# Kernel optimization log

Measured on AMD Instinct MI355X. Metric: run time of the kernel, lower is better.

The kernel has to match this reference:

```python
import jax, jax.numpy as jnp
import numpy as np

B, L, D, H = 2, 256, 256, 4
DH = D // H  # 64


def setup_inputs() -> dict:
    key = jax.random.key(0)
    ks = jax.random.split(key, 20)
    inp = {
        "q": jax.random.normal(ks[0], (B, L, D), jnp.float32),
        "k": jax.random.normal(ks[1], (B, L, D), jnp.float32),
        "v": jax.random.normal(ks[2], (B, L, D), jnp.float32),
        "attn_mask": jnp.zeros((L, L), jnp.float32),  # nonzero => masked
        "key_padding_mask": jnp.zeros((B, L), bool),
        "pitch_rel": jax.random.normal(ks[3], (B, L, L, D), jnp.float32),
        "dur_rel": jax.random.normal(ks[4], (B, L, L, D), jnp.float32),
    }
    scale = 1.0 / np.sqrt(D)
    names = ["Wq", "Wk", "Wv", "fc", "pr", "dr"]
    for i, n in enumerate(names):
        inp[n + "_w"] = jax.random.normal(ks[5 + 2 * i], (D, D), jnp.float32) * scale
        inp[n + "_b"] = jax.random.normal(ks[6 + 2 * i], (D,), jnp.float32) * 0.01
    return inp


def _linear(x, w, b):
    # torch nn.Linear: y = x @ W^T + b
    return jnp.matmul(x, w.T) + b


def reference(q, k, v, attn_mask, key_padding_mask, pitch_rel, dur_rel,
              Wq_w, Wq_b, Wk_w, Wk_b, Wv_w, Wv_b, fc_w, fc_b,
              pr_w, pr_b, dr_w, dr_b):
    Bq, Lq, Dm = q.shape
    Lk = k.shape[1]
    # project and split heads -> (B, H, L, DH)
    def heads(x, w, b):
        return _linear(x, w, b).reshape(Bq, -1, H, DH).transpose(0, 2, 1, 3)
    qh, kh, vh = heads(q, Wq_w, Wq_b), heads(k, Wk_w, Wk_b), heads(v, Wv_w, Wv_b)

    # content scores: (B, H, Lq, Lk)
    logits = jnp.einsum("bhid,bhjd->bhij", qh, kh)

    # relative pitch bias: pitch_rel (B, Lq, Lk, D) -> (B, Lq, Lk, H, DH)
    pr = _linear(pitch_rel, pr_w, pr_b).reshape(Bq, Lq, Lk, H, DH)
    logits = logits + jnp.einsum("bhid,bijhd->bhij", qh, pr)

    dr = _linear(dur_rel, dr_w, dr_b).reshape(Bq, Lq, Lk, H, DH)
    logits = logits + jnp.einsum("bhid,bijhd->bhij", qh, dr)

    logits = logits / np.sqrt(DH)

    # mask: key_padding_mask broadcast over the QUERY axis (as in source),
    # attn_mask nonzero => masked
    mask = jnp.logical_or(key_padding_mask[:, None, :, None],
                          (attn_mask != 0)[None, None, :, :])
    logits = jnp.where(mask, jnp.float32(-9e15), logits)

    attn = jax.nn.softmax(logits, axis=-1)  # (B, H, Lq, Lk)
    out = jnp.einsum("bhij,bhjd->bhid", attn, vh)  # (B, H, Lq, DH)
    out = out.transpose(0, 2, 1, 3).reshape(Bq, Lq, Dm)
    out = _linear(out, fc_w, fc_b)  # dropout is identity in eval mode
    return out, attn
```

## Files before the change

kernel.cpp:

```cpp
#include <hip/hip_runtime.h>
#include <math.h>


__global__ __launch_bounds__(256) void k_transpose(const float* __restrict__ in,
                                                   float* __restrict__ out) {
  __shared__ float t[32][33];
  int bx = blockIdx.x & 7, by = blockIdx.x >> 3;
  int x = threadIdx.x & 31, y0 = threadIdx.x >> 5;
#pragma unroll
  for (int yy = 0; yy < 32; yy += 8)
    t[yy + y0][x] = in[(size_t)(by * 32 + yy + y0) * 256 + bx * 32 + x];
  __syncthreads();
#pragma unroll
  for (int yy = 0; yy < 32; yy += 8)
    out[(size_t)(bx * 32 + yy + y0) * 256 + by * 32 + x] = t[x][yy + y0];
}

__global__ __launch_bounds__(256) void k_proj(
    const float* __restrict__ q, const float* __restrict__ k_, const float* __restrict__ v,
    const float* __restrict__ Wq, const float* __restrict__ Bq,
    const float* __restrict__ Wk, const float* __restrict__ Bk,
    const float* __restrict__ Wv, const float* __restrict__ Bv,
    float* __restrict__ qh, float* __restrict__ kh, float* __restrict__ vh) {
  int blk = blockIdx.x;
  int m = blk >> 5;
  int r = blk & 31;
  int b = r >> 4, it = (r >> 2) & 3, ot = r & 3;
  const float* X = (m == 0) ? q : (m == 1) ? k_ : v;
  const float* W = (m == 0) ? Wq : (m == 1) ? Wk : Wv;
  const float* Bs = (m == 0) ? Bq : (m == 1) ? Bk : Bv;
  float* OUT = (m == 0) ? qh : (m == 1) ? kh : vh;
  const float scale = (m == 0) ? 0.125f : 1.0f;

  __shared__ float xs[64][33];
  __shared__ float ws[64][33];
  int tid = threadIdx.x;
  int ti = tid >> 4, to = tid & 15;
  int lr = tid >> 2, lc = (tid & 3) * 8;
  float acc[4][4] = {};

  for (int k0 = 0; k0 < 256; k0 += 32) {
    float4 a0 = *(const float4*)(X + (size_t)(b * 256 + it * 64 + lr) * 256 + k0 + lc);
    float4 a1 = *(const float4*)(X + (size_t)(b * 256 + it * 64 + lr) * 256 + k0 + lc + 4);
    xs[lr][lc + 0] = a0.x; xs[lr][lc + 1] = a0.y; xs[lr][lc + 2] = a0.z; xs[lr][lc + 3] = a0.w;
    xs[lr][lc + 4] = a1.x; xs[lr][lc + 5] = a1.y; xs[lr][lc + 6] = a1.z; xs[lr][lc + 7] = a1.w;
    float4 w0 = *(const float4*)(W + (size_t)(ot * 64 + lr) * 256 + k0 + lc);
    float4 w1 = *(const float4*)(W + (size_t)(ot * 64 + lr) * 256 + k0 + lc + 4);
    ws[lr][lc + 0] = w0.x; ws[lr][lc + 1] = w0.y; ws[lr][lc + 2] = w0.z; ws[lr][lc + 3] = w0.w;
    ws[lr][lc + 4] = w1.x; ws[lr][lc + 5] = w1.y; ws[lr][lc + 6] = w1.z; ws[lr][lc + 7] = w1.w;
    __syncthreads();
#pragma unroll
    for (int kk = 0; kk < 32; ++kk) {
      float xv0 = xs[ti * 4 + 0][kk], xv1 = xs[ti * 4 + 1][kk];
      float xv2 = xs[ti * 4 + 2][kk], xv3 = xs[ti * 4 + 3][kk];
      float wv0 = ws[0 * 16 + to][kk], wv1 = ws[1 * 16 + to][kk];
      float wv2 = ws[2 * 16 + to][kk], wv3 = ws[3 * 16 + to][kk];
      acc[0][0] += xv0 * wv0; acc[0][1] += xv0 * wv1; acc[0][2] += xv0 * wv2; acc[0][3] += xv0 * wv3;
      acc[1][0] += xv1 * wv0; acc[1][1] += xv1 * wv1; acc[1][2] += xv1 * wv2; acc[1][3] += xv1 * wv3;
      acc[2][0] += xv2 * wv0; acc[2][1] += xv2 * wv1; acc[2][2] += xv2 * wv2; acc[2][3] += xv2 * wv3;
      acc[3][0] += xv3 * wv0; acc[3][1] += xv3 * wv1; acc[3][2] += xv3 * wv2; acc[3][3] += xv3 * wv3;
    }
    __syncthreads();
  }
#pragma unroll
  for (int ii = 0; ii < 4; ++ii)
#pragma unroll
    for (int oo = 0; oo < 4; ++oo) {
      int i = it * 64 + ti * 4 + ii;
      int dd = oo * 16 + to;
      OUT[(size_t)((b * 4 + ot) * 256 + i) * 64 + dd] = (acc[ii][oo] + Bs[ot * 64 + dd]) * scale;
    }
}

__global__ __launch_bounds__(256) void k_qprdr(
    const float* __restrict__ qh, const float* __restrict__ prw,
    const float* __restrict__ drw, float* __restrict__ qpr, float* __restrict__ qdr) {
  int blk = blockIdx.x;
  int t = blk >> 7;
  int r2 = blk & 127;
  int rt = r2 >> 2, et = r2 & 3;
  const float* W = t ? drw : prw;
  float* OUT = t ? qdr : qpr;
  int h = (rt >> 2) & 3;

  __shared__ float xs[64][33];
  __shared__ float ws2[32][64];
  int tid = threadIdx.x;
  int ti = tid >> 4, to = tid & 15;
  float acc[4][4] = {};

  for (int k0 = 0; k0 < 64; k0 += 32) {
    int lr = tid >> 2, lc = (tid & 3) * 8;
    float4 a0 = *(const float4*)(qh + (size_t)(rt * 64 + lr) * 64 + k0 + lc);
    float4 a1 = *(const float4*)(qh + (size_t)(rt * 64 + lr) * 64 + k0 + lc + 4);
    xs[lr][lc + 0] = a0.x; xs[lr][lc + 1] = a0.y; xs[lr][lc + 2] = a0.z; xs[lr][lc + 3] = a0.w;
    xs[lr][lc + 4] = a1.x; xs[lr][lc + 5] = a1.y; xs[lr][lc + 6] = a1.z; xs[lr][lc + 7] = a1.w;
    int wr = tid >> 3, wc = (tid & 7) * 8;
    float4 w0 = *(const float4*)(W + (size_t)(h * 64 + k0 + wr) * 256 + et * 64 + wc);
    float4 w1 = *(const float4*)(W + (size_t)(h * 64 + k0 + wr) * 256 + et * 64 + wc + 4);
    ws2[wr][wc + 0] = w0.x; ws2[wr][wc + 1] = w0.y; ws2[wr][wc + 2] = w0.z; ws2[wr][wc + 3] = w0.w;
    ws2[wr][wc + 4] = w1.x; ws2[wr][wc + 5] = w1.y; ws2[wr][wc + 6] = w1.z; ws2[wr][wc + 7] = w1.w;
    __syncthreads();
#pragma unroll
    for (int kk = 0; kk < 32; ++kk) {
      float xv0 = xs[ti * 4 + 0][kk], xv1 = xs[ti * 4 + 1][kk];
      float xv2 = xs[ti * 4 + 2][kk], xv3 = xs[ti * 4 + 3][kk];
      float wv0 = ws2[kk][0 * 16 + to], wv1 = ws2[kk][1 * 16 + to];
      float wv2 = ws2[kk][2 * 16 + to], wv3 = ws2[kk][3 * 16 + to];
      acc[0][0] += xv0 * wv0; acc[0][1] += xv0 * wv1; acc[0][2] += xv0 * wv2; acc[0][3] += xv0 * wv3;
      acc[1][0] += xv1 * wv0; acc[1][1] += xv1 * wv1; acc[1][2] += xv1 * wv2; acc[1][3] += xv1 * wv3;
      acc[2][0] += xv2 * wv0; acc[2][1] += xv2 * wv1; acc[2][2] += xv2 * wv2; acc[2][3] += xv2 * wv3;
      acc[3][0] += xv3 * wv0; acc[3][1] += xv3 * wv1; acc[3][2] += xv3 * wv2; acc[3][3] += xv3 * wv3;
    }
    __syncthreads();
  }
#pragma unroll
  for (int ii = 0; ii < 4; ++ii)
#pragma unroll
    for (int oo = 0; oo < 4; ++oo)
      OUT[(size_t)(rt * 64 + ti * 4 + ii) * 256 + et * 64 + oo * 16 + to] = acc[ii][oo];
}

__global__ __launch_bounds__(256) void k_qk(const float* __restrict__ qh,
                                            const float* __restrict__ kh,
                                            float* __restrict__ qk) {
  int blk = blockIdx.x;
  int bh = blk >> 4, it = (blk >> 2) & 3, jt = blk & 3;
  __shared__ float xs[64][33];
  __shared__ float ys[64][33];
  int tid = threadIdx.x;
  int ti = tid >> 4, to = tid & 15;
  float acc[4][4] = {};

  for (int k0 = 0; k0 < 64; k0 += 32) {
    int lr = tid >> 2, lc = (tid & 3) * 8;
    float4 a0 = *(const float4*)(qh + (size_t)(bh * 256 + it * 64 + lr) * 64 + k0 + lc);
    float4 a1 = *(const float4*)(qh + (size_t)(bh * 256 + it * 64 + lr) * 64 + k0 + lc + 4);
    xs[lr][lc + 0] = a0.x; xs[lr][lc + 1] = a0.y; xs[lr][lc + 2] = a0.z; xs[lr][lc + 3] = a0.w;
    xs[lr][lc + 4] = a1.x; xs[lr][lc + 5] = a1.y; xs[lr][lc + 6] = a1.z; xs[lr][lc + 7] = a1.w;
    float4 b0 = *(const float4*)(kh + (size_t)(bh * 256 + jt * 64 + lr) * 64 + k0 + lc);
    float4 b1 = *(const float4*)(kh + (size_t)(bh * 256 + jt * 64 + lr) * 64 + k0 + lc + 4);
    ys[lr][lc + 0] = b0.x; ys[lr][lc + 1] = b0.y; ys[lr][lc + 2] = b0.z; ys[lr][lc + 3] = b0.w;
    ys[lr][lc + 4] = b1.x; ys[lr][lc + 5] = b1.y; ys[lr][lc + 6] = b1.z; ys[lr][lc + 7] = b1.w;
    __syncthreads();
#pragma unroll
    for (int kk = 0; kk < 32; ++kk) {
      float xv0 = xs[ti * 4 + 0][kk], xv1 = xs[ti * 4 + 1][kk];
      float xv2 = xs[ti * 4 + 2][kk], xv3 = xs[ti * 4 + 3][kk];
      float wv0 = ys[0 * 16 + to][kk], wv1 = ys[1 * 16 + to][kk];
      float wv2 = ys[2 * 16 + to][kk], wv3 = ys[3 * 16 + to][kk];
      acc[0][0] += xv0 * wv0; acc[0][1] += xv0 * wv1; acc[0][2] += xv0 * wv2; acc[0][3] += xv0 * wv3;
      acc[1][0] += xv1 * wv0; acc[1][1] += xv1 * wv1; acc[1][2] += xv1 * wv2; acc[1][3] += xv1 * wv3;
      acc[2][0] += xv2 * wv0; acc[2][1] += xv2 * wv1; acc[2][2] += xv2 * wv2; acc[2][3] += xv2 * wv3;
      acc[3][0] += xv3 * wv0; acc[3][1] += xv3 * wv1; acc[3][2] += xv3 * wv2; acc[3][3] += xv3 * wv3;
    }
    __syncthreads();
  }
#pragma unroll
  for (int ii = 0; ii < 4; ++ii)
#pragma unroll
    for (int jj = 0; jj < 4; ++jj)
      qk[(size_t)(bh * 256 + it * 64 + ti * 4 + ii) * 256 + jt * 64 + jj * 16 + to] = acc[ii][jj];
}

__global__ __launch_bounds__(256) void k_bias(
    const float* __restrict__ pitch, const float* __restrict__ dur,
    const float* __restrict__ qpr, const float* __restrict__ qdr,
    const float* __restrict__ amask, const unsigned char* __restrict__ kpm,
    float* __restrict__ attn) {
  int blk = blockIdx.x;
  int jc = blk & 3;
  int bi = blk >> 2;
  int b = bi >> 8, i = bi & 255;
  int tid = threadIdx.x, w = tid >> 6, l = tid & 63;

  __shared__ float bias_s[4][64];

  size_t rowbase = (size_t)((b * 4 + w) * 256 + i) * 256 + jc * 64;
  float qkreg = attn[rowbase + l];
  bool maskreg = (kpm[b * 256 + i] != 0) || (amask[(size_t)i * 256 + jc * 64 + l] != 0.f);

  float4 qp[4], qd[4];
#pragma unroll
  for (int h = 0; h < 4; ++h) {
    qp[h] = *(const float4*)(qpr + (size_t)((b * 4 + h) * 256 + i) * 256 + 4 * l);
    qd[h] = *(const float4*)(qdr + (size_t)((b * 4 + h) * 256 + i) * 256 + 4 * l);
  }

  const float4* pbase = (const float4*)(pitch + (size_t)(b * 256 + i) * 65536);
  const float4* dbase = (const float4*)(dur + (size_t)(b * 256 + i) * 65536);

  int j = jc * 64 + w;
  float4 p = pbase[(size_t)j * 64 + l];
  float4 d4 = dbase[(size_t)j * 64 + l];
#pragma unroll 4
  for (int t = 0; t < 16; ++t) {
    float4 pn = make_float4(0.f, 0.f, 0.f, 0.f);
    float4 dn = make_float4(0.f, 0.f, 0.f, 0.f);
    if (t < 15) {
      pn = pbase[(size_t)(j + 4) * 64 + l];
      dn = dbase[(size_t)(j + 4) * 64 + l];
    }
    float s0 = p.x * qp[0].x + p.y * qp[0].y + p.z * qp[0].z + p.w * qp[0].w
             + d4.x * qd[0].x + d4.y * qd[0].y + d4.z * qd[0].z + d4.w * qd[0].w;
    float s1 = p.x * qp[1].x + p.y * qp[1].y + p.z * qp[1].z + p.w * qp[1].w
             + d4.x * qd[1].x + d4.y * qd[1].y + d4.z * qd[1].z + d4.w * qd[1].w;
    float s2 = p.x * qp[2].x + p.y * qp[2].y + p.z * qp[2].z + p.w * qp[2].w
             + d4.x * qd[2].x + d4.y * qd[2].y + d4.z * qd[2].z + d4.w * qd[2].w;
    float s3 = p.x * qp[3].x + p.y * qp[3].y + p.z * qp[3].z + p.w * qp[3].w
             + d4.x * qd[3].x + d4.y * qd[3].y + d4.z * qd[3].z + d4.w * qd[3].w;
    s0 += __shfl_xor(s0, 1); s1 += __shfl_xor(s1, 1);
    s2 += __shfl_xor(s2, 1); s3 += __shfl_xor(s3, 1);
    s0 += __shfl_xor(s0, 2); s1 += __shfl_xor(s1, 2);
    s2 += __shfl_xor(s2, 2); s3 += __shfl_xor(s3, 2);
    int lm = l & 3;
    float a0 = (lm & 1) ? s1 : s0;
    float a1 = (lm & 1) ? s3 : s2;
    float x = (lm & 2) ? a1 : a0;
    x += __shfl_xor(x, 4);
    x += __shfl_xor(x, 8);
    x += __shfl_xor(x, 16);
    x += __shfl_xor(x, 32);
    if (l < 4) bias_s[l][(j & 63)] = x;
    j += 4;
    p = pn;
    d4 = dn;
  }
  __syncthreads();

  float val = qkreg + bias_s[w][l];
  if (maskreg) val = -9e15f;
  attn[rowbase + l] = val;
}

__global__ __launch_bounds__(256) void k_softmax(float* __restrict__ attn) {
  int r = blockIdx.x * 4 + (threadIdx.x >> 6);
  int l = threadIdx.x & 63;
  float* row = attn + (size_t)r * 256;
  float4 v = *(float4*)(row + 4 * l);
  float mx = fmaxf(fmaxf(v.x, v.y), fmaxf(v.z, v.w));
#pragma unroll
  for (int m = 1; m <= 32; m <<= 1) mx = fmaxf(mx, __shfl_xor(mx, m));
  float e0 = __expf(v.x - mx), e1 = __expf(v.y - mx);
  float e2 = __expf(v.z - mx), e3 = __expf(v.w - mx);
  float sm = e0 + e1 + e2 + e3;
#pragma unroll
  for (int m = 1; m <= 32; m <<= 1) sm += __shfl_xor(sm, m);
  float inv = 1.0f / sm;
  *(float4*)(row + 4 * l) = make_float4(e0 * inv, e1 * inv, e2 * inv, e3 * inv);
}

__global__ __launch_bounds__(256) void k_pv_fc(
    const float* __restrict__ attn, const float* __restrict__ vh,
    const float* __restrict__ fcT, const float* __restrict__ fcb,
    float* __restrict__ out) {
  int b = blockIdx.x >> 8, i = blockIdx.x & 255;
  int tid = threadIdx.x;
  int h = tid >> 6, l = tid & 63;

  __shared__ float arow[4][256];
  __shared__ float pre[256];

  *(float4*)&arow[h][4 * l] = *(const float4*)(attn + (size_t)((b * 4 + h) * 256 + i) * 256 + 4 * l);
  __syncthreads();

  float acc = 0.f;
  const float* vbase = vh + (size_t)(b * 4 + h) * 256 * 64 + l;
#pragma unroll 4
  for (int jj = 0; jj < 256; ++jj) acc += arow[h][jj] * vbase[(size_t)jj * 64];
  pre[tid] = acc;
  __syncthreads();

  float acc2 = fcb[tid];
#pragma unroll 4
  for (int c = 0; c < 256; ++c) acc2 += pre[c] * fcT[(size_t)c * 256 + tid];
  out[(size_t)(b * 256 + i) * 256 + tid] = acc2;
}

extern "C" void kernel_launch(void* const* d_in, const int* in_sizes, int n_in,
                              void* d_out, int out_size, void* d_ws, size_t ws_size,
                              hipStream_t stream) {
  (void)in_sizes; (void)n_in; (void)out_size; (void)ws_size;
  const float* q = (const float*)d_in[0];
  const float* k = (const float*)d_in[1];
  const float* v = (const float*)d_in[2];
  const float* amask = (const float*)d_in[3];
  const unsigned char* kpm = (const unsigned char*)d_in[4];
  const float* pitch = (const float*)d_in[5];
  const float* dur = (const float*)d_in[6];
  const float* Wq = (const float*)d_in[7];
  const float* Bq = (const float*)d_in[8];
  const float* Wk = (const float*)d_in[9];
  const float* Bk = (const float*)d_in[10];
  const float* Wv = (const float*)d_in[11];
  const float* Bv = (const float*)d_in[12];
  const float* fcw = (const float*)d_in[13];
  const float* fcb = (const float*)d_in[14];
  const float* prw = (const float*)d_in[15];
  const float* drw = (const float*)d_in[17];

  float* out = (float*)d_out;
  float* attn = out + 2 * 256 * 256;

  float* wsf = (float*)d_ws;
  float* qh = wsf;
  float* kh = qh + 131072;
  float* vh = kh + 131072;
  float* qpr = vh + 131072;
  float* qdr = qpr + 524288;
  float* fcT = qdr + 524288;

  k_transpose<<<64, 256, 0, stream>>>(fcw, fcT);
  k_proj<<<96, 256, 0, stream>>>(q, k, v, Wq, Bq, Wk, Bk, Wv, Bv, qh, kh, vh);
  k_qprdr<<<256, 256, 0, stream>>>(qh, prw, drw, qpr, qdr);
  k_qk<<<128, 256, 0, stream>>>(qh, kh, attn);
  k_bias<<<2048, 256, 0, stream>>>(pitch, dur, qpr, qdr, amask, kpm, attn);
  k_softmax<<<512, 256, 0, stream>>>(attn);
  k_pv_fc<<<512, 256, 0, stream>>>(attn, vh, fcT, fcb, out);
}
```

Measured before the change: 118.8 us.

## Restructure bias kernel with batched loads and LDS reduction; fuse softmax into PV

The bias kernel now has each warp load 8 j-rows of pitch/dur at once (16 float4 loads in flight) instead of a software-pipelined loop of one row at a time. Per-lane partials go to shared memory and are reduced by a transposed read in place of the shuffle reductions, and the grid doubles to 4096 blocks with a launch bound of 3 blocks per CU. Separately, softmax is fused into the PV+fc kernel, which removes one launch and a full read/write pass over attn. The cost is higher register pressure from 32 float4 values per thread and a 33KB shared buffer, which can limit occupancy.

```diff
diff --git a/kernel.cpp b/kernel.cpp
--- a/kernel.cpp
+++ b/kernel.cpp
@@ -163,22 +163,19 @@
       qk[(size_t)(bh * 256 + it * 64 + ti * 4 + ii) * 256 + jt * 64 + jj * 16 + to] = acc[ii][jj];
 }
 
-__global__ __launch_bounds__(256) void k_bias(
+__global__ __launch_bounds__(256, 3) void k_bias(
     const float* __restrict__ pitch, const float* __restrict__ dur,
     const float* __restrict__ qpr, const float* __restrict__ qdr,
     const float* __restrict__ amask, const unsigned char* __restrict__ kpm,
     float* __restrict__ attn) {
   int blk = blockIdx.x;
-  int jc = blk & 3;
-  int bi = blk >> 2;
+  int jc = blk & 7;
+  int bi = blk >> 3;
   int b = bi >> 8, i = bi & 255;
   int tid = threadIdx.x, w = tid >> 6, l = tid & 63;
-
-  __shared__ float bias_s[4][64];
-
-  size_t rowbase = (size_t)((b * 4 + w) * 256 + i) * 256 + jc * 64;
-  float qkreg = attn[rowbase + l];
-  bool maskreg = (kpm[b * 256 + i] != 0) || (amask[(size_t)i * 256 + jc * 64 + l] != 0.f);
+  int jb = jc * 32 + w * 8;
+
+  __shared__ float red[4][8][4][65];
 
   float4 qp[4], qd[4];
 #pragma unroll
@@ -187,71 +184,52 @@
     qd[h] = *(const float4*)(qdr + (size_t)((b * 4 + h) * 256 + i) * 256 + 4 * l);
   }
 
-  const float4* pbase = (const float4*)(pitch + (size_t)(b * 256 + i) * 65536);
-  const float4* dbase = (const float4*)(dur + (size_t)(b * 256 + i) * 65536);
-
-  int j = jc * 64 + w;
-  float4 p = pbase[(size_t)j * 64 + l];
-  float4 d4 = dbase[(size_t)j * 64 + l];
-#pragma unroll 4
-  for (int t = 0; t < 16; ++t) {
-    float4 pn = make_float4(0.f, 0.f, 0.f, 0.f);
-    float4 dn = make_float4(0.f, 0.f, 0.f, 0.f);
-    if (t < 15) {
-      pn = pbase[(size_t)(j + 4) * 64 + l];
-      dn = dbase[(size_t)(j + 4) * 64 + l];
-    }
-    float s0 = p.x * qp[0].x + p.y * qp[0].y + p.z * qp[0].z + p.w * qp[0].w
-             + d4.x * qd[0].x + d4.y * qd[0].y + d4.z * qd[0].z + d4.w * qd[0].w;
-    float s1 = p.x * qp[1].x + p.y * qp[1].y + p.z * qp[1].z + p.w * qp[1].w
-             + d4.x * qd[1].x + d4.y * qd[1].y + d4.z * qd[1].z + d4.w * qd[1].w;
-    float s2 = p.x * qp[2].x + p.y * qp[2].y + p.z * qp[2].z + p.w * qp[2].w
-             + d4.x * qd[2].x + d4.y * qd[2].y + d4.z * qd[2].z + d4.w * qd[2].w;
-    float s3 = p.x * qp[3].x + p.y * qp[3].y + p.z * qp[3].z + p.w * qp[3].w
-             + d4.x * qd[3].x + d4.y * qd[3].y + d4.z * qd[3].z + d4.w * qd[3].w;
-    s0 += __shfl_xor(s0, 1); s1 += __shfl_xor(s1, 1);
-    s2 += __shfl_xor(s2, 1); s3 += __shfl_xor(s3, 1);
-    s0 += __shfl_xor(s0, 2); s1 += __shfl_xor(s1, 2);
-    s2 += __shfl_xor(s2, 2); s3 += __shfl_xor(s3, 2);
-    int lm = l & 3;
-    float a0 = (lm & 1) ? s1 : s0;
-    float a1 = (lm & 1) ? s3 : s2;
-    float x = (lm & 2) ? a1 : a0;
-    x += __shfl_xor(x, 4);
-    x += __shfl_xor(x, 8);
-    x += __shfl_xor(x, 16);
-    x += __shfl_xor(x, 32);
-    if (l < 4) bias_s[l][(j & 63)] = x;
-    j += 4;
-    p = pn;
-    d4 = dn;
-  }
-  __syncthreads();
-
-  float val = qkreg + bias_s[w][l];
-  if (maskreg) val = -9e15f;
-  attn[rowbase + l] = val;
-}
-
-__global__ __launch_bounds__(256) void k_softmax(float* __restrict__ attn) {
-  int r = blockIdx.x * 4 + (threadIdx.x >> 6);
-  int l = threadIdx.x & 63;
-  float* row = attn + (size_t)r * 256;
-  float4 v = *(float4*)(row + 4 * l);
-  float mx = fmaxf(fmaxf(v.x, v.y), fmaxf(v.z, v.w));
-#pragma unroll
-  for (int m = 1; m <= 32; m <<= 1) mx = fmaxf(mx, __shfl_xor(mx, m));
-  float e0 = __expf(v.x - mx), e1 = __expf(v.y - mx);
-  float e2 = __expf(v.z - mx), e3 = __expf(v.w - mx);
-  float sm = e0 + e1 + e2 + e3;
-#pragma unroll
-  for (int m = 1; m <= 32; m <<= 1) sm += __shfl_xor(sm, m);
-  float inv = 1.0f / sm;
-  *(float4*)(row + 4 * l) = make_float4(e0 * inv, e1 * inv, e2 * inv, e3 * inv);
+  int p = l & 31;
+  int jj_o = p >> 2, h_o = p & 3;
+  int jabs = jb + jj_o;
+  size_t orow = (size_t)((b * 4 + h_o) * 256 + i) * 256 + jabs;
+  float qkreg = attn[orow];
+  bool maskreg = (kpm[b * 256 + i] != 0) || (amask[(size_t)i * 256 + jabs] != 0.f);
+
+  const float4* prow = (const float4*)(pitch + ((size_t)(b * 256 + i) * 256 + jb) * 256);
+  const float4* drow = (const float4*)(dur + ((size_t)(b * 256 + i) * 256 + jb) * 256);
+
+  float4 P[8], D[8];
+#pragma unroll
+  for (int g = 0; g < 8; ++g) P[g] = prow[(size_t)g * 64 + l];
+#pragma unroll
+  for (int g = 0; g < 8; ++g) D[g] = drow[(size_t)g * 64 + l];
+
+  float acc[8][4];
+#pragma unroll
+  for (int jj = 0; jj < 8; ++jj)
+#pragma unroll
+    for (int h = 0; h < 4; ++h)
+      acc[jj][h] = P[jj].x * qp[h].x + P[jj].y * qp[h].y + P[jj].z * qp[h].z + P[jj].w * qp[h].w
+                 + D[jj].x * qd[h].x + D[jj].y * qd[h].y + D[jj].z * qd[h].z + D[jj].w * qd[h].w;
+
+#pragma unroll
+  for (int jj = 0; jj < 8; ++jj)
+#pragma unroll
+    for (int h = 0; h < 4; ++h)
+      red[w][jj][h][l] = acc[jj][h];
+
+  int half = l >> 5;
+  const float* rrow = &red[w][jj_o][h_o][0];
+  float x = 0.f;
+#pragma unroll
+  for (int c = 0; c < 32; ++c) x += rrow[half * 32 + c];
+  x += __shfl_xor(x, 32);
+
+  if (l < 32) {
+    float val = qkreg + x;
+    if (maskreg) val = -9e15f;
+    attn[orow] = val;
+  }
 }
 
 __global__ __launch_bounds__(256) void k_pv_fc(
-    const float* __restrict__ attn, const float* __restrict__ vh,
+    float* __restrict__ attn, const float* __restrict__ vh,
     const float* __restrict__ fcT, const float* __restrict__ fcb,
     float* __restrict__ out) {
   int b = blockIdx.x >> 8, i = blockIdx.x & 255;
@@ -261,7 +239,20 @@
   __shared__ float arow[4][256];
   __shared__ float pre[256];
 
-  *(float4*)&arow[h][4 * l] = *(const float4*)(attn + (size_t)((b * 4 + h) * 256 + i) * 256 + 4 * l);
+  float* rowp = attn + (size_t)((b * 4 + h) * 256 + i) * 256;
+  float4 v4 = *(float4*)(rowp + 4 * l);
+  float mx = fmaxf(fmaxf(v4.x, v4.y), fmaxf(v4.z, v4.w));
+#pragma unroll
+  for (int m = 1; m <= 32; m <<= 1) mx = fmaxf(mx, __shfl_xor(mx, m));
+  float e0 = __expf(v4.x - mx), e1 = __expf(v4.y - mx);
+  float e2 = __expf(v4.z - mx), e3 = __expf(v4.w - mx);
+  float sm = e0 + e1 + e2 + e3;
+#pragma unroll
+  for (int m = 1; m <= 32; m <<= 1) sm += __shfl_xor(sm, m);
+  float inv = 1.0f / sm;
+  float4 a4 = make_float4(e0 * inv, e1 * inv, e2 * inv, e3 * inv);
+  *(float4*)(rowp + 4 * l) = a4;
+  *(float4*)&arow[h][4 * l] = a4;
   __syncthreads();
 
   float acc = 0.f;
@@ -314,7 +305,6 @@
   k_proj<<<96, 256, 0, stream>>>(q, k, v, Wq, Bq, Wk, Bk, Wv, Bv, qh, kh, vh);
   k_qprdr<<<256, 256, 0, stream>>>(qh, prw, drw, qpr, qdr);
   k_qk<<<128, 256, 0, stream>>>(qh, kh, attn);
-  k_bias<<<2048, 256, 0, stream>>>(pitch, dur, qpr, qdr, amask, kpm, attn);
-  k_softmax<<<512, 256, 0, stream>>>(attn);
+  k_bias<<<4096, 256, 0, stream>>>(pitch, dur, qpr, qdr, amask, kpm, attn);
   k_pv_fc<<<512, 256, 0, stream>>>(attn, vh, fcT, fcb, out);
 }
```

Result: no change. 117.0 us (-1.5%).
